# Kernel optimization log

Hardware: AMD Instinct MI355X
Metric: run time of the kernel (lower is better)

## Reference

```python
import jax, jax.numpy as jnp
import numpy as np

EMBED_DIM = 512
SMOOTH = 4.0        # args.lambda_softmax
LAMBDA_LSE = 6.0    # args.lambda_lse
LEAKY_SLOPE = 0.1
EPS = 1e-8


def setup_inputs() -> dict:
    key = jax.random.key(0)
    k1, k2, k3 = jax.random.split(key, 3)
    n_contract, n_region = 32, 256
    n_law, max_len = 32, 256
    contracts = jax.random.normal(k1, (n_contract, n_region, EMBED_DIM), jnp.float32)
    laws = jax.random.normal(k2, (n_law, max_len, EMBED_DIM), jnp.float32)
    law_lens = jax.random.randint(k3, (n_law,), 128, max_len + 1, jnp.int32)
    return {"contracts": contracts, "laws": laws, "law_lens": law_lens}


def reference(contracts, laws, law_lens):
    # contracts: [C, R, D], laws: [N, L, D], law_lens: [N]
    n_law, max_len, d = laws.shape
    # mask[n, l] = 1 if word l is within law n's true length
    mask = (jnp.arange(max_len)[None, :] < law_lens[:, None]).astype(contracts.dtype)

    # attn = law @ contract^T / sqrt(D): [N, C, L, R]
    attn = jnp.einsum('nld,crd->nclr', laws, contracts) / jnp.sqrt(jnp.float32(d))
    attn = jax.nn.leaky_relu(attn, LEAKY_SLOPE)
    # l2norm over region dim (per law-word row)
    attn = attn / (jnp.linalg.norm(attn, axis=-1, keepdims=True) + EPS)
    attn = jax.nn.softmax(attn, axis=-1) * SMOOTH
    # zero out contributions from padded law words (ragged lengths)
    attn = attn * mask[:, None, :, None]

    # weighted_law: [N, C, R, D]
    wlaw = jnp.einsum('nld,nclr->ncrd', laws, attn)

    # cosine similarity along D: [N, C, R]
    w12 = jnp.sum(contracts[None] * wlaw, axis=-1)
    w1 = jnp.linalg.norm(contracts, axis=-1)[None]          # [1, C, R]
    w2 = jnp.linalg.norm(wlaw, axis=-1)                      # [N, C, R]
    sim = w12 / jnp.maximum(w1 * w2, EPS)

    # LogSumExp aggregation over regions -> [N, C]
    row_sim = jnp.log(jnp.sum(jnp.exp(sim * LAMBDA_LSE), axis=-1)) / LAMBDA_LSE
    # concatenate per-law columns -> [C, N]
    return row_sim.T
```

## Files before the change

kernel.cpp:

```cpp
#include <hip/hip_runtime.h>
#include <hip/hip_bf16.h>

#define CN 32
#define RN 256
#define DN 512
#define NN 32
#define LN 256

#define STAGE_OFF 131072
#define SMEM_TOTAL 163840

typedef short v8s __attribute__((ext_vector_type(8)));
typedef float v4f __attribute__((ext_vector_type(4)));
typedef const __attribute__((address_space(1))) void* gas1_t;
typedef __attribute__((address_space(3))) void* las3_t;

__device__ __forceinline__ void gl2lds16(const void* g, void* l) {
  __builtin_amdgcn_global_load_lds((gas1_t)g, (las3_t)l, 16, 0, 0);
}

__device__ __forceinline__ unsigned short f2bf(float x) {
  unsigned int u = __float_as_uint(x);
  u = (u + 0x7fffu + ((u >> 16) & 1u)) >> 16;
  return (unsigned short)u;
}
__device__ __forceinline__ float bf2f(unsigned short h) {
  return __uint_as_float(((unsigned int)h) << 16);
}

__device__ __forceinline__ const v8s* stgFrag(const unsigned short* buf, int r,
                                              int quad) {
  return (const v8s*)(buf + r * 32 + ((quad ^ ((r >> 1) & 3)) << 3));
}

__device__ __forceinline__ int satIdx(int r, int col) {
  return (r << 8) | ((((col >> 3) ^ (r & 7)) << 3) | (col & 7));
}

__global__ __launch_bounds__(256) void prep_kernel(
    const float* __restrict__ con, const float* __restrict__ laws,
    unsigned short* __restrict__ lawsB, unsigned short* __restrict__ conB,
    float* __restrict__ cnorm) {
  const int bid = blockIdx.x;
  const int t = threadIdx.x;
  if (bid < 2048) {
    const int r = bid * 4 + (t >> 6);
    const int lane = t & 63;
    const float4* src = (const float4*)(con + r * DN + lane * 8);
    float4 x0 = src[0], x1 = src[1];
    unsigned short h[8];
    h[0] = f2bf(x0.x); h[1] = f2bf(x0.y); h[2] = f2bf(x0.z); h[3] = f2bf(x0.w);
    h[4] = f2bf(x1.x); h[5] = f2bf(x1.y); h[6] = f2bf(x1.z); h[7] = f2bf(x1.w);
    *(v8s*)(conB + r * DN + lane * 8) = *(v8s*)h;
    float s = x0.x * x0.x + x0.y * x0.y + x0.z * x0.z + x0.w * x0.w +
              x1.x * x1.x + x1.y * x1.y + x1.z * x1.z + x1.w * x1.w;
#pragma unroll
    for (int m = 1; m < 64; m <<= 1) s += __shfl_xor(s, m, 64);
    if (lane == 0) cnorm[r] = sqrtf(s);
  } else {
    const int off = (bid - 2048) * 2048 + t * 8;
    const float4* src = (const float4*)(laws + off);
    float4 x0 = src[0], x1 = src[1];
    unsigned short h[8];
    h[0] = f2bf(x0.x); h[1] = f2bf(x0.y); h[2] = f2bf(x0.z); h[3] = f2bf(x0.w);
    h[4] = f2bf(x1.x); h[5] = f2bf(x1.y); h[6] = f2bf(x1.z); h[7] = f2bf(x1.w);
    *(v8s*)(lawsB + off) = *(v8s*)h;
  }
}

__global__ __launch_bounds__(512) void gramm_kernel(
    const unsigned short* __restrict__ lawsB, unsigned short* __restrict__ G) {
  __shared__ unsigned short slice[256 * 32];
  const int bx = blockIdx.x;
  const int n = bx >> 3;
  const int m0 = (bx & 7) << 5;
  const int t = threadIdx.x;
  const int lane = t & 63;
  const int w = t >> 6;
  const int quad = lane >> 4;
  const int l16 = lane & 15;
  const int sub = t & 3;
  const int rQ = t >> 2;
  const int subx = sub ^ ((rQ >> 1) & 3);
  const int rg = w >> 2;
  const int cg = w & 3;
  const unsigned short* lawN = lawsB + n * (LN * DN);

  v4f acc[4];
#pragma unroll
  for (int b = 0; b < 4; ++b) acc[b] = (v4f){0.f, 0.f, 0.f, 0.f};

  for (int ch = 0; ch < 16; ++ch) {
    const int dk = ch << 5;
    __syncthreads();
#pragma unroll
    for (int i = 0; i < 2; ++i)
      gl2lds16(lawN + (i * 128 + rQ) * DN + dk + subx * 8,
               (char*)slice + i * 8192 + t * 16);
    __syncthreads();
    v8s af = *stgFrag(slice, m0 + rg * 16 + l16, quad);
#pragma unroll
    for (int ct = 0; ct < 4; ++ct) {
      v8s bf = *stgFrag(slice, cg * 64 + ct * 16 + l16, quad);
      acc[ct] = __builtin_amdgcn_mfma_f32_16x16x32_bf16(af, bf, acc[ct], 0, 0, 0);
    }
  }
  unsigned short* g = G + n * (LN * LN);
#pragma unroll
  for (int ct = 0; ct < 4; ++ct)
#pragma unroll
    for (int reg = 0; reg < 4; ++reg) {
      const int l = m0 + rg * 16 + quad * 4 + reg;
      g[l * LN + cg * 64 + ct * 16 + l16] = f2bf(acc[ct][reg]);
    }
}

__global__ __launch_bounds__(512, 2) void main_kernel(
    const int* __restrict__ law_lens, const unsigned short* __restrict__ lawsB,
    const unsigned short* __restrict__ conB, const unsigned short* __restrict__ Gm,
    const float* __restrict__ cnorm, float* __restrict__ out) {
  extern __shared__ char smem[];
  unsigned short* sAt = (unsigned short*)smem;
  char* stage = smem + STAGE_OFF;

  const int bid = blockIdx.x;
  const int n = bid >> 5;
  const int c = bid & 31;
  const int t = threadIdx.x;
  const int lane = t & 63;
  const int w = t >> 6;
  const int quad = lane >> 4;
  const int l16 = lane & 15;
  const int sub = t & 3;
  const int rQ = t >> 2;
  const int subx = sub ^ ((rQ >> 1) & 3);
  const int len = law_lens[n];
  const bool active = (w * 32) < len;
  const int nCh = (len + 31) >> 5;

  const unsigned short* lawN = lawsB + n * (LN * DN);
  const unsigned short* conC = conB + c * (RN * DN);
  const unsigned short* Gn = Gm + n * (LN * LN);

  float w12p[16];
#pragma unroll
  for (int i = 0; i < 16; ++i) w12p[i] = 0.f;

  {
    const unsigned short* a0p = lawN + (w * 32 + l16) * DN + quad * 8;
    const unsigned short* a1p = a0p + 16 * DN;

    v4f acc[2][16];
#pragma unroll
    for (int a = 0; a < 2; ++a)
#pragma unroll
      for (int b = 0; b < 16; ++b) acc[a][b] = (v4f){0.f, 0.f, 0.f, 0.f};

#pragma unroll
    for (int i = 0; i < 2; ++i)
      gl2lds16(conC + (i * 128 + rQ) * DN + subx * 8,
               stage + i * 8192 + t * 16);

    for (int ch = 0; ch < 16; ++ch) {
      const int dk = ch << 5;
      __syncthreads();
      v8s af0, af1;
      if (active) {
        af0 = *(const v8s*)(a0p + dk);
        af1 = *(const v8s*)(a1p + dk);
      }
      __builtin_amdgcn_sched_barrier(0);
      if (ch < 15) {
        char* dst = stage + ((ch + 1) & 1) * 16384;
#pragma unroll
        for (int i = 0; i < 2; ++i)
          gl2lds16(conC + (i * 128 + rQ) * DN + (dk + 32) + subx * 8,
                   dst + i * 8192 + t * 16);
      }
      __builtin_amdgcn_sched_barrier(0);
      if (active) {
        const unsigned short* cs =
            (const unsigned short*)(stage + (ch & 1) * 16384);
#pragma unroll
        for (int rt = 0; rt < 16; ++rt) {
          v8s bf = *stgFrag(cs, rt * 16 + l16, quad);
          acc[0][rt] = __builtin_amdgcn_mfma_f32_16x16x32_bf16(af0, bf, acc[0][rt], 0, 0, 0);
          acc[1][rt] = __builtin_amdgcn_mfma_f32_16x16x32_bf16(af1, bf, acc[1][rt], 0, 0, 0);
        }
      }
    }
    if (active) {
#pragma unroll
      for (int tl = 0; tl < 2; ++tl) {
        unsigned int pk[16][2];
#pragma unroll
        for (int reg = 0; reg < 4; ++reg) {
          const int lg = w * 32 + tl * 16 + quad * 4 + reg;
          float v[16], lv[16];
          float ss = 0.f;
#pragma unroll
          for (int rt = 0; rt < 16; ++rt) {
            v[rt] = acc[tl][rt][reg] * 0.04419417382415922f;
            lv[rt] = v[rt] > 0.f ? v[rt] : 0.1f * v[rt];
            ss += lv[rt] * lv[rt];
          }
#pragma unroll
          for (int m = 1; m < 16; m <<= 1) ss += __shfl_xor(ss, m, 64);
          const float inv = 1.f / (sqrtf(ss) + 1e-8f);
          float e[16];
          float den = 0.f;
#pragma unroll
          for (int rt = 0; rt < 16; ++rt) {
            e[rt] = __expf(lv[rt] * inv);
            den += e[rt];
          }
#pragma unroll
          for (int m = 1; m < 16; m <<= 1) den += __shfl_xor(den, m, 64);
          const float sc = (lg < len) ? 4.f / den : 0.f;
#pragma unroll
          for (int rt = 0; rt < 16; ++rt) {
            const float a = e[rt] * sc;
            w12p[rt] += a * v[rt];
            const unsigned int h = f2bf(a);
            if (reg & 1)
              pk[rt][reg >> 1] |= h << 16;
            else
              pk[rt][reg >> 1] = h;
          }
        }
        const int lg0 = w * 32 + tl * 16 + quad * 4;
#pragma unroll
        for (int rt = 0; rt < 16; ++rt)
          *(uint2*)(sAt + satIdx(rt * 16 + l16, lg0)) = *(uint2*)pk[rt];
      }
    }
  }

  __syncthreads();

#pragma unroll
  for (int i = 0; i < 2; ++i)
    gl2lds16(Gn + (i * 128 + rQ) * LN + subx * 8, stage + i * 8192 + t * 16);

#pragma unroll
  for (int rt = 0; rt < 16; ++rt) {
    w12p[rt] += __shfl_xor(w12p[rt], 16, 64);
    w12p[rt] += __shfl_xor(w12p[rt], 32, 64);
  }

  float nsv[2][4];
  {
    v4f acc[2][16];
#pragma unroll
    for (int a = 0; a < 2; ++a)
#pragma unroll
      for (int b = 0; b < 16; ++b) acc[a][b] = (v4f){0.f, 0.f, 0.f, 0.f};

    for (int ch = 0; ch < nCh; ++ch) {
      const int lk = ch << 5;
      __syncthreads();
      v8s af0 = *(const v8s*)(sAt + satIdx(w * 32 + l16, lk + quad * 8));
      v8s af1 = *(const v8s*)(sAt + satIdx(w * 32 + 16 + l16, lk + quad * 8));
      __builtin_amdgcn_sched_barrier(0);
      if (ch < nCh - 1) {
        char* dst = stage + ((ch + 1) & 1) * 16384;
#pragma unroll
        for (int i = 0; i < 2; ++i)
          gl2lds16(Gn + (i * 128 + rQ) * LN + (lk + 32) + subx * 8,
                   dst + i * 8192 + t * 16);
      }
      __builtin_amdgcn_sched_barrier(0);
      const unsigned short* gs =
          (const unsigned short*)(stage + (ch & 1) * 16384);
#pragma unroll
      for (int lt = 0; lt < 16; ++lt) {
        if ((lt << 4) < len) {
          v8s bf = *stgFrag(gs, lt * 16 + l16, quad);
          acc[0][lt] = __builtin_amdgcn_mfma_f32_16x16x32_bf16(af0, bf, acc[0][lt], 0, 0, 0);
          acc[1][lt] = __builtin_amdgcn_mfma_f32_16x16x32_bf16(af1, bf, acc[1][lt], 0, 0, 0);
        }
      }
    }
#pragma unroll
    for (int tl = 0; tl < 2; ++tl) {
#pragma unroll
      for (int reg = 0; reg < 4; ++reg) {
        const int r = w * 32 + tl * 16 + quad * 4 + reg;
        float s = 0.f;
#pragma unroll
        for (int lt = 0; lt < 16; ++lt)
          if ((lt << 4) < len)
            s += acc[tl][lt][reg] * bf2f(sAt[satIdx(r, lt * 16 + l16)]);
#pragma unroll
        for (int m = 1; m < 16; m <<= 1) s += __shfl_xor(s, m, 64);
        nsv[tl][reg] = s;
      }
    }
  }

  float* w12s = (float*)stage;
  float* nsqS = (float*)(stage + 8192);
  float* red = (float*)(stage + 9216);
  __syncthreads();
  if (l16 == 0) {
#pragma unroll
    for (int tl = 0; tl < 2; ++tl)
#pragma unroll
      for (int reg = 0; reg < 4; ++reg)
        nsqS[w * 32 + tl * 16 + quad * 4 + reg] = nsv[tl][reg];
  }
  if (lane < 16) {
#pragma unroll
    for (int rt = 0; rt < 16; ++rt) w12s[w * 256 + rt * 16 + lane] = w12p[rt];
  }
  __syncthreads();
  float p = 0.f;
  if (t < 256) {
    float w12 = 0.f;
#pragma unroll
    for (int i = 0; i < 8; ++i) w12 += w12s[i * 256 + t];
    const float w1 = cnorm[c * RN + t];
    const float w2 = sqrtf(fmaxf(nsqS[t], 0.f));
    const float sim = (w12 * 22.627416997969522f) / fmaxf(w1 * w2, 1e-8f);
    p = __expf(6.f * sim);
  }
#pragma unroll
  for (int m = 1; m < 64; m <<= 1) p += __shfl_xor(p, m, 64);
  if (lane == 0) red[w] = p;
  __syncthreads();
  if (t == 0) {
    float s = 0.f;
#pragma unroll
    for (int i = 0; i < 8; ++i) s += red[i];
    out[c * NN + n] = logf(s) / 6.f;
  }
}

extern "C" void kernel_launch(void* const* d_in, const int* in_sizes, int n_in,
                              void* d_out, int out_size, void* d_ws, size_t ws_size,
                              hipStream_t stream) {
  (void)in_sizes; (void)n_in; (void)out_size;
  const float* contracts = (const float*)d_in[0];
  const float* laws = (const float*)d_in[1];
  const int* law_lens = (const int*)d_in[2];
  float* out = (float*)d_out;

  unsigned short* lawsB = (unsigned short*)d_ws;
  unsigned short* conB = lawsB + NN * LN * DN;
  unsigned short* G = conB + CN * RN * DN;
  float* cnorm = (float*)(G + NN * LN * LN);
  if (ws_size < (size_t)21004288) return;

  hipFuncSetAttribute((const void*)main_kernel,
                      hipFuncAttributeMaxDynamicSharedMemorySize, SMEM_TOTAL);

  prep_kernel<<<4096, 256, 0, stream>>>(contracts, laws, lawsB, conB, cnorm);
  gramm_kernel<<<256, 512, 0, stream>>>(lawsB, G);
  main_kernel<<<1024, 512, SMEM_TOTAL, stream>>>(law_lens, lawsB, conB, G,
                                                 cnorm, out);
}
```

Measured before the change: 260.3 us.

## Fuse prep and Gram kernels into one launch; drop ragged-length skip branches

Merges the bf16 conversion kernel and the law Gram-matrix kernel into a single setup kernel. The Gram blocks now read fp32 laws directly into LDS with a rotated layout and convert to bf16 on fragment load, which removes the dependency on the converted laws and one kernel launch. The main kernel also drops the per-wave 'active' guards and the per-tile length checks, so it does uniform MFMA work on padded rows. That trades extra math for simpler, branch-free scheduling.

```diff
diff --git a/kernel.cpp b/kernel.cpp
--- a/kernel.cpp
+++ b/kernel.cpp
@@ -37,14 +37,69 @@
   return (r << 8) | ((((col >> 3) ^ (r & 7)) << 3) | (col & 7));
 }
 
-__global__ __launch_bounds__(256) void prep_kernel(
+__device__ __forceinline__ v8s ldFrag32(const float* buf, int r, int quad) {
+  const float* p = buf + r * 32 + (((quad + r) & 3) << 3);
+  const float4 x0 = ((const float4*)p)[0];
+  const float4 x1 = ((const float4*)p)[1];
+  unsigned short h[8];
+  h[0] = f2bf(x0.x); h[1] = f2bf(x0.y); h[2] = f2bf(x0.z); h[3] = f2bf(x0.w);
+  h[4] = f2bf(x1.x); h[5] = f2bf(x1.y); h[6] = f2bf(x1.z); h[7] = f2bf(x1.w);
+  return *(v8s*)h;
+}
+
+__global__ __launch_bounds__(512) void setup_kernel(
     const float* __restrict__ con, const float* __restrict__ laws,
     unsigned short* __restrict__ lawsB, unsigned short* __restrict__ conB,
-    float* __restrict__ cnorm) {
+    float* __restrict__ cnorm, unsigned short* __restrict__ G) {
   const int bid = blockIdx.x;
   const int t = threadIdx.x;
-  if (bid < 2048) {
-    const int r = bid * 4 + (t >> 6);
+  if (bid < 256) {
+    __shared__ float slice[256 * 32];
+    const int n = bid >> 3;
+    const int m0 = (bid & 7) << 5;
+    const int lane = t & 63;
+    const int w = t >> 6;
+    const int quad = lane >> 4;
+    const int l16 = lane & 15;
+    const int rg = w >> 2;
+    const int cg = w & 3;
+    const float* lawN = laws + n * (LN * DN);
+    const int srow = t >> 3;
+    const int sc4 = (t >> 1) & 3;
+    const int shalf = t & 1;
+
+    v4f acc[4];
+#pragma unroll
+    for (int b = 0; b < 4; ++b) acc[b] = (v4f){0.f, 0.f, 0.f, 0.f};
+
+    for (int ch = 0; ch < 16; ++ch) {
+      const int dk = ch << 5;
+      __syncthreads();
+#pragma unroll
+      for (int i = 0; i < 4; ++i) {
+        const int row = i * 64 + srow;
+        const int srcCol = (((sc4 - row) & 3) << 3) + (shalf << 2);
+        gl2lds16(lawN + row * DN + dk + srcCol,
+                 (char*)slice + i * 8192 + t * 16);
+      }
+      __syncthreads();
+      v8s af = ldFrag32(slice, m0 + rg * 16 + l16, quad);
+#pragma unroll
+      for (int ct = 0; ct < 4; ++ct) {
+        v8s bf = ldFrag32(slice, cg * 64 + ct * 16 + l16, quad);
+        acc[ct] = __builtin_amdgcn_mfma_f32_16x16x32_bf16(af, bf, acc[ct], 0, 0, 0);
+      }
+    }
+    unsigned short* g = G + n * (LN * LN);
+#pragma unroll
+    for (int ct = 0; ct < 4; ++ct)
+#pragma unroll
+      for (int reg = 0; reg < 4; ++reg) {
+        const int l = m0 + rg * 16 + quad * 4 + reg;
+        g[l * LN + cg * 64 + ct * 16 + l16] = f2bf(acc[ct][reg]);
+      }
+  } else if (bid < 1280) {
+    const int r = (bid - 256) * 8 + (t >> 6);
     const int lane = t & 63;
     const float4* src = (const float4*)(con + r * DN + lane * 8);
     float4 x0 = src[0], x1 = src[1];
@@ -58,7 +113,7 @@
     for (int m = 1; m < 64; m <<= 1) s += __shfl_xor(s, m, 64);
     if (lane == 0) cnorm[r] = sqrtf(s);
   } else {
-    const int off = (bid - 2048) * 2048 + t * 8;
+    const int off = (bid - 1280) * 4096 + t * 8;
     const float4* src = (const float4*)(laws + off);
     float4 x0 = src[0], x1 = src[1];
     unsigned short h[8];
@@ -66,53 +121,6 @@
     h[4] = f2bf(x1.x); h[5] = f2bf(x1.y); h[6] = f2bf(x1.z); h[7] = f2bf(x1.w);
     *(v8s*)(lawsB + off) = *(v8s*)h;
   }
-}
-
-__global__ __launch_bounds__(512) void gramm_kernel(
-    const unsigned short* __restrict__ lawsB, unsigned short* __restrict__ G) {
-  __shared__ unsigned short slice[256 * 32];
-  const int bx = blockIdx.x;
-  const int n = bx >> 3;
-  const int m0 = (bx & 7) << 5;
-  const int t = threadIdx.x;
-  const int lane = t & 63;
-  const int w = t >> 6;
-  const int quad = lane >> 4;
-  const int l16 = lane & 15;
-  const int sub = t & 3;
-  const int rQ = t >> 2;
-  const int subx = sub ^ ((rQ >> 1) & 3);
-  const int rg = w >> 2;
-  const int cg = w & 3;
-  const unsigned short* lawN = lawsB + n * (LN * DN);
-
-  v4f acc[4];
-#pragma unroll
-  for (int b = 0; b < 4; ++b) acc[b] = (v4f){0.f, 0.f, 0.f, 0.f};
-
-  for (int ch = 0; ch < 16; ++ch) {
-    const int dk = ch << 5;
-    __syncthreads();
-#pragma unroll
-    for (int i = 0; i < 2; ++i)
-      gl2lds16(lawN + (i * 128 + rQ) * DN + dk + subx * 8,
-               (char*)slice + i * 8192 + t * 16);
-    __syncthreads();
-    v8s af = *stgFrag(slice, m0 + rg * 16 + l16, quad);
-#pragma unroll
-    for (int ct = 0; ct < 4; ++ct) {
-      v8s bf = *stgFrag(slice, cg * 64 + ct * 16 + l16, quad);
-      acc[ct] = __builtin_amdgcn_mfma_f32_16x16x32_bf16(af, bf, acc[ct], 0, 0, 0);
-    }
-  }
-  unsigned short* g = G + n * (LN * LN);
-#pragma unroll
-  for (int ct = 0; ct < 4; ++ct)
-#pragma unroll
-    for (int reg = 0; reg < 4; ++reg) {
-      const int l = m0 + rg * 16 + quad * 4 + reg;
-      g[l * LN + cg * 64 + ct * 16 + l16] = f2bf(acc[ct][reg]);
-    }
 }
 
 __global__ __launch_bounds__(512, 2) void main_kernel(
@@ -135,7 +143,6 @@
   const int rQ = t >> 2;
   const int subx = sub ^ ((rQ >> 1) & 3);
   const int len = law_lens[n];
-  const bool active = (w * 32) < len;
   const int nCh = (len + 31) >> 5;
 
   const unsigned short* lawN = lawsB + n * (LN * DN);
@@ -164,11 +171,8 @@
     for (int ch = 0; ch < 16; ++ch) {
       const int dk = ch << 5;
       __syncthreads();
-      v8s af0, af1;
-      if (active) {
-        af0 = *(const v8s*)(a0p + dk);
-        af1 = *(const v8s*)(a1p + dk);
-      }
+      v8s af0 = *(const v8s*)(a0p + dk);
+      v8s af1 = *(const v8s*)(a1p + dk);
       __builtin_amdgcn_sched_barrier(0);
       if (ch < 15) {
         char* dst = stage + ((ch + 1) & 1) * 16384;
@@ -178,61 +182,57 @@
                    dst + i * 8192 + t * 16);
       }
       __builtin_amdgcn_sched_barrier(0);
-      if (active) {
-        const unsigned short* cs =
-            (const unsigned short*)(stage + (ch & 1) * 16384);
+      const unsigned short* cs =
+          (const unsigned short*)(stage + (ch & 1) * 16384);
+#pragma unroll
+      for (int rt = 0; rt < 16; ++rt) {
+        v8s bf = *stgFrag(cs, rt * 16 + l16, quad);
+        acc[0][rt] = __builtin_amdgcn_mfma_f32_16x16x32_bf16(af0, bf, acc[0][rt], 0, 0, 0);
+        acc[1][rt] = __builtin_amdgcn_mfma_f32_16x16x32_bf16(af1, bf, acc[1][rt], 0, 0, 0);
+      }
+    }
+#pragma unroll
+    for (int tl = 0; tl < 2; ++tl) {
+      unsigned int pk[16][2];
+#pragma unroll
+      for (int reg = 0; reg < 4; ++reg) {
+        const int lg = w * 32 + tl * 16 + quad * 4 + reg;
+        float v[16], lv[16];
+        float ss = 0.f;
 #pragma unroll
         for (int rt = 0; rt < 16; ++rt) {
-          v8s bf = *stgFrag(cs, rt * 16 + l16, quad);
-          acc[0][rt] = __builtin_amdgcn_mfma_f32_16x16x32_bf16(af0, bf, acc[0][rt], 0, 0, 0);
-          acc[1][rt] = __builtin_amdgcn_mfma_f32_16x16x32_bf16(af1, bf, acc[1][rt], 0, 0, 0);
+          v[rt] = acc[tl][rt][reg] * 0.04419417382415922f;
+          lv[rt] = v[rt] > 0.f ? v[rt] : 0.1f * v[rt];
+          ss += lv[rt] * lv[rt];
         }
-      }
-    }
-    if (active) {
-#pragma unroll
-      for (int tl = 0; tl < 2; ++tl) {
-        unsigned int pk[16][2];
-#pragma unroll
-        for (int reg = 0; reg < 4; ++reg) {
-          const int lg = w * 32 + tl * 16 + quad * 4 + reg;
-          float v[16], lv[16];
-          float ss = 0.f;
-#pragma unroll
-          for (int rt = 0; rt < 16; ++rt) {
-            v[rt] = acc[tl][rt][reg] * 0.04419417382415922f;
-            lv[rt] = v[rt] > 0.f ? v[rt] : 0.1f * v[rt];
-            ss += lv[rt] * lv[rt];
-          }
-#pragma unroll
-          for (int m = 1; m < 16; m <<= 1) ss += __shfl_xor(ss, m, 64);
-          const float inv = 1.f / (sqrtf(ss) + 1e-8f);
-          float e[16];
-          float den = 0.f;
-#pragma unroll
-          for (int rt = 0; rt < 16; ++rt) {
-            e[rt] = __expf(lv[rt] * inv);
-            den += e[rt];
-          }
-#pragma unroll
-          for (int m = 1; m < 16; m <<= 1) den += __shfl_xor(den, m, 64);
-          const float sc = (lg < len) ? 4.f / den : 0.f;
-#pragma unroll
-          for (int rt = 0; rt < 16; ++rt) {
-            const float a = e[rt] * sc;
-            w12p[rt] += a * v[rt];
-            const unsigned int h = f2bf(a);
-            if (reg & 1)
-              pk[rt][reg >> 1] |= h << 16;
-            else
-              pk[rt][reg >> 1] = h;
-          }
+#pragma unroll
+        for (int m = 1; m < 16; m <<= 1) ss += __shfl_xor(ss, m, 64);
+        const float inv = 1.f / (sqrtf(ss) + 1e-8f);
+        float e[16];
+        float den = 0.f;
+#pragma unroll
+        for (int rt = 0; rt < 16; ++rt) {
+          e[rt] = __expf(lv[rt] * inv);
+          den += e[rt];
         }
-        const int lg0 = w * 32 + tl * 16 + quad * 4;
-#pragma unroll
-        for (int rt = 0; rt < 16; ++rt)
-          *(uint2*)(sAt + satIdx(rt * 16 + l16, lg0)) = *(uint2*)pk[rt];
-      }
+#pragma unroll
+        for (int m = 1; m < 16; m <<= 1) den += __shfl_xor(den, m, 64);
+        const float sc = (lg < len) ? 4.f / den : 0.f;
+#pragma unroll
+        for (int rt = 0; rt < 16; ++rt) {
+          const float a = e[rt] * sc;
+          w12p[rt] += a * v[rt];
+          const unsigned int h = f2bf(a);
+          if (reg & 1)
+            pk[rt][reg >> 1] |= h << 16;
+          else
+            pk[rt][reg >> 1] = h;
+        }
+      }
+      const int lg0 = w * 32 + tl * 16 + quad * 4;
+#pragma unroll
+      for (int rt = 0; rt < 16; ++rt)
+        *(uint2*)(sAt + satIdx(rt * 16 + l16, lg0)) = *(uint2*)pk[rt];
     }
   }
 
@@ -274,11 +274,9 @@
           (const unsigned short*)(stage + (ch & 1) * 16384);
 #pragma unroll
       for (int lt = 0; lt < 16; ++lt) {
-        if ((lt << 4) < len) {
-          v8s bf = *stgFrag(gs, lt * 16 + l16, quad);
-          acc[0][lt] = __builtin_amdgcn_mfma_f32_16x16x32_bf16(af0, bf, acc[0][lt], 0, 0, 0);
-          acc[1][lt] = __builtin_amdgcn_mfma_f32_16x16x32_bf16(af1, bf, acc[1][lt], 0, 0, 0);
-        }
+        v8s bf = *stgFrag(gs, lt * 16 + l16, quad);
+        acc[0][lt] = __builtin_amdgcn_mfma_f32_16x16x32_bf16(af0, bf, acc[0][lt], 0, 0, 0);
+        acc[1][lt] = __builtin_amdgcn_mfma_f32_16x16x32_bf16(af1, bf, acc[1][lt], 0, 0, 0);
       }
     }
 #pragma unroll
@@ -289,8 +287,7 @@
         float s = 0.f;
 #pragma unroll
         for (int lt = 0; lt < 16; ++lt)
-          if ((lt << 4) < len)
-            s += acc[tl][lt][reg] * bf2f(sAt[satIdx(r, lt * 16 + l16)]);
+          s += acc[tl][lt][reg] * bf2f(sAt[satIdx(r, lt * 16 + l16)]);
 #pragma unroll
         for (int m = 1; m < 16; m <<= 1) s += __shfl_xor(s, m, 64);
         nsv[tl][reg] = s;
@@ -354,8 +351,8 @@
   hipFuncSetAttribute((const void*)main_kernel,
                       hipFuncAttributeMaxDynamicSharedMemorySize, SMEM_TOTAL);
 
-  prep_kernel<<<4096, 256, 0, stream>>>(contracts, laws, lawsB, conB, cnorm);
-  gramm_kernel<<<256, 512, 0, stream>>>(lawsB, G);
+  setup_kernel<<<2304, 512, 0, stream>>>(contracts, laws, lawsB, conB, cnorm,
+                                         G);
   main_kernel<<<1024, 512, SMEM_TOTAL, stream>>>(law_lens, lawsB, conB, G,
                                                  cnorm, out);
 }
```

Result: faster. 247.9 us (-4.7%).
